# Kernel tuning notes

Measured on AMD Instinct MI355X. Metric: run time of the kernel, lower is better.

Reference implementation:

```python
import jax, jax.numpy as jnp
import numpy as np

B, T, D = 8, 2048, 512
S = 4                 # n_slots
SLOT_DIM = D          # cfg.slot_dim defaults to d_model
SE = 8                # state_embed_dim
GH = 64               # gate_hidden
EMA = 0.99
SIGMA_FLOOR = 1e-3
OPEN2CLOSING, CLOSING2LOCKED, UNLOCK = 0.1, 0.03, 0.25
GAINS = jnp.array([1.0, 0.5, 0.1], dtype=jnp.float32)  # OPEN, CLOSING, LOCKED


def _glorot(k, shape, fi, fo):
    b = (6.0 / (fi + fo)) ** 0.5
    return jax.random.uniform(k, shape, jnp.float32, -b, b)


def setup_inputs() -> dict:
    key = jax.random.key(0)
    ks = jax.random.split(key, 8)
    gate_in = D + 1 + SE  # [h, z, state_embed]
    return {
        'h_seq': jax.random.normal(ks[0], (B, T, D), jnp.float32),
        'pred_W': _glorot(ks[1], (S, D, D), D, D),
        'pred_b': jnp.zeros((S, D), jnp.float32),
        'gate_W1': _glorot(ks[2], (S, gate_in, GH), gate_in, GH),
        'gate_b1': jnp.zeros((S, GH), jnp.float32),
        'gate_W2': _glorot(ks[3], (S, GH, 1), GH, 1),
        'gate_b2': jnp.zeros((S, 1), jnp.float32),
        'write_W': _glorot(ks[4], (S, D, SLOT_DIM), D, SLOT_DIM),
        'write_b': jnp.zeros((S, SLOT_DIM), jnp.float32),
        'w0': jnp.zeros((S, SLOT_DIM), jnp.float32),
        'state_embed': jax.random.normal(ks[5], (3, SE), jnp.float32),
    }


def reference(h_seq, pred_W, pred_b, gate_W1, gate_b1, gate_W2, gate_b2,
              write_W, write_b, w0, state_embed):
    Bb, Tt, Dd = h_seq.shape
    h_det = jax.lax.stop_gradient(h_seq)
    # per-slot next-step predictions (input detached, as in torch): (B,T,S,D)
    preds = jnp.einsum('btd,sdo->btso', h_det, pred_W) + pred_b
    # prediction emitted at t-1 targets h_t
    pred_prev = jnp.concatenate([jnp.zeros_like(preds[:, :1]), preds[:, :-1]], axis=1)
    valid = jnp.arange(Tt) > 0  # no surprise signal at t=0

    m0 = jnp.broadcast_to(w0, (Bb, S, SLOT_DIM)).astype(h_seq.dtype)
    carry0 = (m0,
              jnp.zeros((S,), jnp.float32),       # mu
              jnp.ones((S,), jnp.float32),        # sigma
              jnp.full((S,), 0.5, jnp.float32),   # gate_ema
              jnp.zeros((S,), jnp.int32))         # slot_state

    def step(carry, xs):
        m, mu, sigma, gate_ema, state = carry
        h_t, p_prev, ok = xs  # (B,D), (B,S,D), scalar bool
        # prediction-error surprise per slot
        err = jnp.sqrt(jnp.sum((p_prev - h_t[:, None, :]) ** 2, axis=-1) + 1e-8)  # (B,S)
        err = jnp.where(ok, err, 0.0)
        z = (err - mu) / jnp.maximum(sigma, SIGMA_FLOOR)  # (B,S)
        # gate MLP over [h, z, state_embed]
        se = state_embed[state]  # (S,SE)
        gin = jnp.concatenate([
            jnp.broadcast_to(h_t[:, None, :], (Bb, S, Dd)),
            z[..., None],
            jnp.broadcast_to(se[None], (Bb, S, SE))], axis=-1)
        hid = jax.nn.relu(jnp.einsum('bsi,sih->bsh', gin, gate_W1) + gate_b1)
        g = jax.nn.sigmoid(jnp.einsum('bsh,sho->bso', hid, gate_W2) + gate_b2)[..., 0]  # (B,S)
        # state-dependent write gain (OPEN/CLOSING/LOCKED)
        g_eff = g * GAINS[state]
        w_enc = jnp.einsum('bd,sdo->bso', h_t, write_W) + write_b
        m = (1.0 - g_eff[..., None]) * m + g_eff[..., None] * w_enc
        read = m.reshape(Bb, S * SLOT_DIM)
        # homeostatic bookkeeping (buffers: non-differentiable, EMA)
        err_s = jax.lax.stop_gradient(err)
        mu_n = jnp.where(ok, EMA * mu + (1 - EMA) * err_s.mean(0), mu)
        sigma_n = jnp.where(ok, EMA * sigma + (1 - EMA) * jnp.abs(err_s - mu).mean(0), sigma)
        gate_ema_n = EMA * gate_ema + (1 - EMA) * jax.lax.stop_gradient(g).mean(0)
        # state machine transitions on gate EMA
        st = jnp.where((state == 0) & (gate_ema_n < OPEN2CLOSING), 1, state)
        st = jnp.where((state == 1) & (gate_ema_n < CLOSING2LOCKED), 2,
             jnp.where((state == 1) & (gate_ema_n > UNLOCK), 0, st))
        st = jnp.where((state == 2) & (gate_ema_n > UNLOCK), 0, st)
        return (m, mu_n, sigma_n, gate_ema_n, st), read

    xs = (jnp.swapaxes(h_seq, 0, 1), jnp.swapaxes(pred_prev, 0, 1), valid)
    _, reads = jax.lax.scan(step, carry0, xs)
    return jnp.swapaxes(reads, 0, 1)  # (B,T,S*SLOT_DIM)
```

## Files before the change

### kernel.cpp

```cpp
#include <hip/hip_runtime.h>
#include <hip/hip_bf16.h>

#define Bb 8
#define Tt 2048
#define Dd 512
#define Ss 4
#define GHh 64
#define NCHUNK 64
#define CH 32

typedef __hip_bfloat16 bf16;
typedef short bf16x8 __attribute__((ext_vector_type(8)));
typedef float f32x4 __attribute__((ext_vector_type(4)));
__device__ __forceinline__ float b2f(bf16 x){ return __bfloat162float(x); }

#define GLOAD_LDS16(g, l) \
  __builtin_amdgcn_global_load_lds((const __attribute__((address_space(1))) unsigned int*)(const void*)(g), \
                                   (__attribute__((address_space(3))) unsigned int*)(l), 16, 0, 0)

__global__ __launch_bounds__(256) void k0a_cvt(const float* __restrict__ h, bf16* __restrict__ hb){
  int i = (blockIdx.x*256 + threadIdx.x)*4;
  float4 v = *reinterpret_cast<const float4*>(&h[i]);
  hb[i+0] = __float2bfloat16(v.x);
  hb[i+1] = __float2bfloat16(v.y);
  hb[i+2] = __float2bfloat16(v.z);
  hb[i+3] = __float2bfloat16(v.w);
}

__global__ __launch_bounds__(256) void k0b_pack(const float* __restrict__ predW,
    const float* __restrict__ writeW, const float* __restrict__ gateW1, bf16* __restrict__ Wt){
  __shared__ float tile[32][33];
  int k0 = blockIdx.x*32, n0 = blockIdx.y*32;
  int tx = threadIdx.x & 31, ty = threadIdx.x >> 5;
  #pragma unroll
  for (int p = 0; p < 4; ++p) {
    int kk = ty + p*8;
    int n = n0 + tx, k = k0 + kk;
    float v;
    if (n < 2048)      { int s=n>>9, o=n&511;              v = predW[((size_t)s*512+k)*512+o]; }
    else if (n < 4096) { int n2=n-2048; int s=n2>>9,o=n2&511; v = writeW[((size_t)s*512+k)*512+o]; }
    else               { int n2=n-4096; int s=n2>>6,hh=n2&63; v = gateW1[((size_t)s*521+k)*64+hh]; }
    tile[kk][tx] = v;
  }
  __syncthreads();
  #pragma unroll
  for (int p = 0; p < 4; ++p) {
    int nn = ty + p*8;
    Wt[(size_t)(n0+nn)*512 + k0 + tx] = __float2bfloat16(tile[tx][nn]);
  }
}

__global__ __launch_bounds__(256) void k1_mfma(
    const bf16* __restrict__ hb, const bf16* __restrict__ Wt,
    const float* __restrict__ h, const float* __restrict__ predb, const float* __restrict__ writeb,
    bf16* __restrict__ wenc, float* __restrict__ hg, float* __restrict__ errsq)
{
  __shared__ bf16 As[2][128*64];
  __shared__ bf16 Bs[2][128*64];
  const int tid = threadIdx.x;
  const int w = tid >> 6, lane = tid & 63;
  const int n0 = blockIdx.x * 128;
  const int row0 = blockIdx.y * 128;
  const int wm = w & 1, wn = w >> 1;
  const int mrow = lane & 15, kq = lane >> 4;

  f32x4 acc[4][4];
  #pragma unroll
  for (int i=0;i<4;++i)
    #pragma unroll
    for (int j=0;j<4;++j) acc[i][j] = (f32x4){0.f,0.f,0.f,0.f};

  const int srow  = lane >> 3;
  const int sslot = (lane & 7) ^ srow;
  const bf16* gaBase = hb + (size_t)(row0 + w*32 + srow)*512 + sslot*8;
  const bf16* gbBase = Wt + (size_t)(n0  + w*32 + srow)*512 + sslot*8;

  auto STAGE = [&](int buf, int kstep){
    const bf16* ga = gaBase + kstep*64;
    const bf16* gb = gbBase + kstep*64;
    bf16* lA = &As[buf][(w*32)*64];
    bf16* lB = &Bs[buf][(w*32)*64];
    #pragma unroll
    for (int i=0;i<4;++i) {
      GLOAD_LDS16(ga + (size_t)i*8*512, lA + i*8*64);
      GLOAD_LDS16(gb + (size_t)i*8*512, lB + i*8*64);
    }
  };

  auto COMPUTE = [&](int buf){
    #pragma unroll
    for (int kk=0; kk<2; ++kk) {
      bf16x8 af[4], bfr[4];
      #pragma unroll
      for (int mi=0;mi<4;++mi) {
        int r = wm*64 + mi*16 + mrow;
        af[mi] = *reinterpret_cast<const bf16x8*>(&As[buf][r*64 + (((kk*4+kq) ^ (r&7))<<3)]);
      }
      #pragma unroll
      for (int ni=0;ni<4;++ni) {
        int r = wn*64 + ni*16 + mrow;
        bfr[ni] = *reinterpret_cast<const bf16x8*>(&Bs[buf][r*64 + (((kk*4+kq) ^ (r&7))<<3)]);
      }
      #pragma unroll
      for (int mi=0;mi<4;++mi)
        #pragma unroll
        for (int ni=0;ni<4;++ni)
          acc[mi][ni] = __builtin_amdgcn_mfma_f32_16x16x32_bf16(af[mi], bfr[ni], acc[mi][ni], 0, 0, 0);
    }
  };

  STAGE(0, 0);
  __syncthreads();
  #pragma unroll
  for (int t = 0; t < 8; ++t) {
    if (t < 7) STAGE((t+1)&1, t+1);
    COMPUTE(t&1);
    __syncthreads();
  }

  if (n0 < 2048) {
    const int s = n0 >> 9;
    #pragma unroll
    for (int mi=0;mi<4;++mi) {
      #pragma unroll
      for (int reg=0;reg<4;++reg) {
        int r = row0 + wm*64 + mi*16 + kq*4 + reg;
        float sum = 0.f;
        if ((r & 2047) != 2047) {
          #pragma unroll
          for (int ni=0;ni<4;++ni) {
            int o = (n0 & 511) + wn*64 + ni*16 + mrow;
            float P = acc[mi][ni][reg] + predb[s*512 + o];
            float d = P - h[(size_t)(r+1)*512 + o];
            sum = fmaf(d, d, sum);
          }
        }
        #pragma unroll
        for (int off=1; off<16; off<<=1) sum += __shfl_xor(sum, off);
        if (mrow == 0 && (r & 2047) != 2047)
          atomicAdd(&errsq[(size_t)(r+1)*4 + s], sum);
      }
    }
  } else if (n0 < 4096) {
    #pragma unroll
    for (int mi=0;mi<4;++mi)
      #pragma unroll
      for (int ni=0;ni<4;++ni) {
        int n2 = n0 - 2048 + wn*64 + ni*16 + mrow;
        int s = n2 >> 9, o = n2 & 511;
        float wb = writeb[s*512 + o];
        #pragma unroll
        for (int reg=0;reg<4;++reg) {
          int r = row0 + wm*64 + mi*16 + kq*4 + reg;
          wenc[((size_t)r*4 + s)*512 + o] = __float2bfloat16(acc[mi][ni][reg] + wb);
        }
      }
  } else {
    #pragma unroll
    for (int mi=0;mi<4;++mi)
      #pragma unroll
      for (int ni=0;ni<4;++ni) {
        int n2 = n0 - 4096 + wn*64 + ni*16 + mrow;
        int s = n2 >> 6, hh = n2 & 63;
        #pragma unroll
        for (int reg=0;reg<4;++reg) {
          int r = row0 + wm*64 + mi*16 + kq*4 + reg;
          hg[((size_t)r*4 + s)*64 + hh] = acc[mi][ni][reg];
        }
      }
  }
}

__global__ void k2a_err(const float* __restrict__ errsq, float* __restrict__ err){
  int i = blockIdx.x*256 + threadIdx.x;
  int t = (i >> 2) & 2047;
  err[i] = (t > 0) ? sqrtf(errsq[i] + 1e-8f) : 0.f;
}

__global__ void k2b_em(const float* __restrict__ err, float* __restrict__ em){
  int i = blockIdx.x*256 + threadIdx.x;
  float sum = 0.f;
  #pragma unroll
  for (int b=0;b<8;++b) sum += err[b*8192 + i];
  em[i] = sum * 0.125f;
}

__global__ void k2c_scan(const float* __restrict__ in, float* __restrict__ outv, float init){
  __shared__ float s_in[8192];
  for (int i = threadIdx.x; i < 8192; i += 256) s_in[i] = in[i];
  __syncthreads();
  if (threadIdx.x < 4) {
    int s = threadIdx.x;
    float v = init;
    for (int t = 0; t < 2048; ++t) {
      outv[t*4+s] = v;
      if (t >= 1) v = 0.99f*v + 0.01f*s_in[t*4+s];
    }
  }
}

__global__ void k2d_sd(const float* __restrict__ err, const float* __restrict__ MU, float* __restrict__ sd){
  int i = blockIdx.x*256 + threadIdx.x;
  float mu = MU[i];
  float sum = 0.f;
  #pragma unroll
  for (int b=0;b<8;++b) sum += fabsf(err[b*8192 + i] - mu);
  sd[i] = sum * 0.125f;
}

__global__ void k2e_base(const float* __restrict__ gateW1, const float* __restrict__ semb,
                         const float* __restrict__ gateb1, float* __restrict__ base1){
  int i = blockIdx.x*256 + threadIdx.x;
  if (i < 768) {
    int hh = i & 63, k = (i >> 6) % 3, s = i / 192;
    float acc = gateb1[s*64 + hh];
    #pragma unroll
    for (int e = 0; e < 8; ++e)
      acc = fmaf(semb[k*8+e], gateW1[((size_t)s*521 + 513 + e)*64 + hh], acc);
    base1[i] = acc;
  }
}

__global__ void k3_gall(const float* __restrict__ hg, const float* __restrict__ err,
    const float* __restrict__ MU, const float* __restrict__ SIG,
    const float* __restrict__ gateW1, const float* __restrict__ base1,
    const float* __restrict__ gateW2, const float* __restrict__ gateb2,
    float* __restrict__ g_all)
{
  int i = blockIdx.x*256 + threadIdx.x;
  int k = i % 3;
  int bts = i / 3;
  int s = bts & 3;
  int t = (bts >> 2) & 2047;
  float e = err[bts];
  float z = (e - MU[t*4+s]) / fmaxf(SIG[t*4+s], 1e-3f);
  const float* hgp = &hg[(size_t)bts*64];
  const float* b1p = &base1[(s*3 + k)*64];
  const float* w1zp = &gateW1[((size_t)s*521 + 512)*64];
  const float* w2p = &gateW2[s*64];
  float logit = 0.f;
  for (int hh = 0; hh < 64; ++hh) {
    float hid = hgp[hh] + z*w1zp[hh] + b1p[hh];
    hid = fmaxf(hid, 0.f);
    logit = fmaf(hid, w2p[hh], logit);
  }
  logit += gateb2[s];
  g_all[i] = 1.f/(1.f + expf(-logit));
}

__global__ void k3b_gm(const float* __restrict__ g_all, float* __restrict__ gm){
  int i = blockIdx.x*256 + threadIdx.x;
  float sum = 0.f;
  #pragma unroll
  for (int b=0;b<8;++b) sum += g_all[((size_t)b*8192 + i/3)*3 + (i%3)];
  gm[i] = sum * 0.125f;
}

__global__ void k4_scan(const float* __restrict__ gm, int* __restrict__ states){
  __shared__ float s_gm[6144];
  float ema = 0.5f; int st = 0;
  for (int c = 0; c < 4; ++c) {
    __syncthreads();
    for (int i = threadIdx.x; i < 6144; i += 256) s_gm[i] = gm[c*6144 + i];
    __syncthreads();
    if (threadIdx.x < 4) {
      int s = threadIdx.x;
      for (int tt = 0; tt < 512; ++tt) {
        int t = c*512 + tt;
        states[t*4+s] = st;
        float g = s_gm[tt*12 + s*3 + st];
        ema = 0.99f*ema + 0.01f*g;
        int ns = st;
        if (st == 0 && ema < 0.1f) ns = 1;
        if (st == 1) ns = (ema < 0.03f) ? 2 : ((ema > 0.25f) ? 0 : 1);
        if (st == 2 && ema > 0.25f) ns = 0;
        st = ns;
      }
    }
  }
}

__global__ void k5_a(const float* __restrict__ g_all, const int* __restrict__ states, float* __restrict__ a){
  int i = blockIdx.x*256 + threadIdx.x;
  int ts = i & 8191;
  int st = states[ts];
  float gain = (st == 0) ? 1.f : ((st == 1) ? 0.5f : 0.1f);
  a[i] = g_all[(size_t)i*3 + st] * gain;
}

__global__ __launch_bounds__(64) void k6_pass1(const float* __restrict__ a, const bf16* __restrict__ wenc,
      float* __restrict__ q, float* __restrict__ Pc){
  int c = blockIdx.x, s = blockIdx.y, b = blockIdx.z;
  int d0 = threadIdx.x << 3;
  __shared__ float s_a[CH];
  if (threadIdx.x < CH) s_a[threadIdx.x] = a[(size_t)(b*2048 + c*CH + threadIdx.x)*4 + s];
  __syncthreads();
  float qv[8];
  #pragma unroll
  for (int j=0;j<8;++j) qv[j] = 0.f;
  float p = 1.f;
  const bf16* wp = &wenc[((size_t)(b*2048 + c*CH)*4 + s)*512 + d0];
  #pragma unroll 4
  for (int i = 0; i < CH; ++i) {
    float av = s_a[i];
    bf16x8 wv = *reinterpret_cast<const bf16x8*>(wp + (size_t)i*4*512);
    float om = 1.f - av;
    #pragma unroll
    for (int j=0;j<8;++j) qv[j] = fmaf(om, qv[j], av*b2f(((const bf16*)&wv)[j]));
    p *= om;
  }
  float* qp = &q[((size_t)(b*4+s)*NCHUNK + c)*512 + d0];
  #pragma unroll
  for (int j=0;j<8;++j) qp[j] = qv[j];
  if (threadIdx.x == 0) Pc[(b*4+s)*NCHUNK + c] = p;
}

__global__ __launch_bounds__(512) void k7_bound(const float* __restrict__ q, const float* __restrict__ Pc,
      const float* __restrict__ w0, float* __restrict__ m_start){
  int s = blockIdx.x, b = blockIdx.y, d = threadIdx.x;
  float m = w0[s*512 + d];
  for (int c = 0; c < NCHUNK; ++c) {
    m_start[((size_t)(b*4+s)*NCHUNK + c)*512 + d] = m;
    m = Pc[(b*4+s)*NCHUNK + c]*m + q[((size_t)(b*4+s)*NCHUNK + c)*512 + d];
  }
}

__global__ __launch_bounds__(64) void k8_pass2(const float* __restrict__ a, const bf16* __restrict__ wenc,
      const float* __restrict__ m_start, float* __restrict__ out){
  int c = blockIdx.x, s = blockIdx.y, b = blockIdx.z;
  int d0 = threadIdx.x << 3;
  __shared__ float s_a[CH];
  if (threadIdx.x < CH) s_a[threadIdx.x] = a[(size_t)(b*2048 + c*CH + threadIdx.x)*4 + s];
  __syncthreads();
  float m[8];
  const float* msp = &m_start[((size_t)(b*4+s)*NCHUNK + c)*512 + d0];
  #pragma unroll
  for (int j=0;j<8;++j) m[j] = msp[j];
  const bf16* wp = &wenc[((size_t)(b*2048 + c*CH)*4 + s)*512 + d0];
  float* op = &out[((size_t)(b*2048 + c*CH))*2048 + s*512 + d0];
  #pragma unroll 2
  for (int i = 0; i < CH; ++i) {
    float av = s_a[i];
    bf16x8 wv = *reinterpret_cast<const bf16x8*>(wp + (size_t)i*4*512);
    float om = 1.f - av;
    #pragma unroll
    for (int j=0;j<8;++j) m[j] = fmaf(om, m[j], av*b2f(((const bf16*)&wv)[j]));
    #pragma unroll
    for (int j=0;j<8;++j) op[(size_t)i*2048 + j] = m[j];
  }
}

extern "C" void kernel_launch(void* const* d_in, const int* in_sizes, int n_in,
                              void* d_out, int out_size, void* d_ws, size_t ws_size,
                              hipStream_t stream) {
  (void)in_sizes; (void)n_in; (void)out_size; (void)ws_size;
  const float* h      = (const float*)d_in[0];
  const float* predW  = (const float*)d_in[1];
  const float* predb  = (const float*)d_in[2];
  const float* gateW1 = (const float*)d_in[3];
  const float* gateb1 = (const float*)d_in[4];
  const float* gateW2 = (const float*)d_in[5];
  const float* gateb2 = (const float*)d_in[6];
  const float* writeW = (const float*)d_in[7];
  const float* writeb = (const float*)d_in[8];
  const float* w0     = (const float*)d_in[9];
  const float* semb   = (const float*)d_in[10];
  float* out = (float*)d_out;

  char* ws = (char*)d_ws;
  size_t off = 0;
  auto alloc = [&](size_t bytes) -> char* {
    char* p = ws + off; off += (bytes + 255) / 256 * 256; return p;
  };
  bf16*  wenc   = (bf16*) alloc((size_t)Bb*Tt*Ss*Dd*2);
  float* hg     = (float*)alloc((size_t)Bb*Tt*Ss*GHh*4);
  bf16*  hb     = (bf16*) alloc((size_t)Bb*Tt*Dd*2);
  bf16*  Wt     = (bf16*) alloc((size_t)4352*512*2);
  float* errsq  = (float*)alloc((size_t)Bb*Tt*Ss*4);
  float* err    = (float*)alloc((size_t)Bb*Tt*Ss*4);
  float* em     = (float*)alloc((size_t)Tt*Ss*4);
  float* MU     = (float*)alloc((size_t)Tt*Ss*4);
  float* sd     = (float*)alloc((size_t)Tt*Ss*4);
  float* SIG    = (float*)alloc((size_t)Tt*Ss*4);
  float* base1  = (float*)alloc((size_t)Ss*3*GHh*4);
  float* g_all  = (float*)alloc((size_t)Bb*Tt*Ss*3*4);
  float* gm     = (float*)alloc((size_t)Tt*Ss*3*4);
  int*   states = (int*)  alloc((size_t)Tt*Ss*4);
  float* av     = (float*)alloc((size_t)Bb*Tt*Ss*4);
  float* Pc     = (float*)alloc((size_t)Bb*Ss*NCHUNK*4);
  float* q      = (float*)alloc((size_t)Bb*Ss*NCHUNK*Dd*4);
  float* mst    = (float*)alloc((size_t)Bb*Ss*NCHUNK*Dd*4);

  hipMemsetAsync(errsq, 0, (size_t)Bb*Tt*Ss*4, stream);

  k0a_cvt<<<(Bb*Tt*Dd)/(256*4), 256, 0, stream>>>(h, hb);
  dim3 g0b(16, 136);
  k0b_pack<<<g0b, 256, 0, stream>>>(predW, writeW, gateW1, Wt);
  dim3 g1(34, 128);
  k1_mfma<<<g1, 256, 0, stream>>>(hb, Wt, h, predb, writeb, wenc, hg, errsq);
  k2a_err<<<(Bb*Tt*Ss)/256, 256, 0, stream>>>(errsq, err);
  k2b_em<<<(Tt*Ss)/256, 256, 0, stream>>>(err, em);
  k2c_scan<<<1, 256, 0, stream>>>(em, MU, 0.f);
  k2d_sd<<<(Tt*Ss)/256, 256, 0, stream>>>(err, MU, sd);
  k2c_scan<<<1, 256, 0, stream>>>(sd, SIG, 1.f);
  k2e_base<<<3, 256, 0, stream>>>(gateW1, semb, gateb1, base1);
  k3_gall<<<(Bb*Tt*Ss*3)/256, 256, 0, stream>>>(hg, err, MU, SIG, gateW1, base1, gateW2, gateb2, g_all);
  k3b_gm<<<(Tt*Ss*3)/256, 256, 0, stream>>>(g_all, gm);
  k4_scan<<<1, 256, 0, stream>>>(gm, states);
  k5_a<<<(Bb*Tt*Ss)/256, 256, 0, stream>>>(g_all, states, av);
  dim3 g6(NCHUNK, Ss, Bb);
  k6_pass1<<<g6, 64, 0, stream>>>(av, wenc, q, Pc);
  dim3 g7(Ss, Bb);
  k7_bound<<<g7, 512, 0, stream>>>(q, Pc, w0, mst);
  k8_pass2<<<g6, 64, 0, stream>>>(av, wenc, mst, out);
}
```

Before: 646.5 us.

## Parallelize EMA scan into chunks and shorten state-machine dependency chain

The mu/sigma EMA scan kernel becomes a three-phase chunked linear scan: 256 threads each reduce a 32-step chunk to an affine (A,B) pair, four threads combine the chunk prefixes, then every thread replays its chunk to write outputs. This replaces a 2048-step serial loop that ran on four threads. The gate-EMA state-machine scan, which must stay serial, now double-buffers its shared-memory staging so the next chunk loads while the current one runs. Its loop body computes all three candidate EMAs and next states before selecting, which takes the branchy state-dependent load off the critical path. Computing A as a power of 0.99 and reordering the FMAs may change float rounding slightly.

```diff
diff --git a/kernel.cpp b/kernel.cpp
--- a/kernel.cpp
+++ b/kernel.cpp
@@ -185,17 +185,35 @@
   em[i] = sum * 0.125f;
 }
 
-__global__ void k2c_scan(const float* __restrict__ in, float* __restrict__ outv, float init){
+__global__ __launch_bounds__(256) void k2c_scan(const float* __restrict__ in, float* __restrict__ outv, float init){
   __shared__ float s_in[8192];
+  __shared__ float sA[256], sB[256], s_entry[256];
   for (int i = threadIdx.x; i < 8192; i += 256) s_in[i] = in[i];
   __syncthreads();
+  const int c = threadIdx.x >> 2, s = threadIdx.x & 3;
+  float A = 1.f, B = 0.f;
+  #pragma unroll 8
+  for (int i = 0; i < 32; ++i) {
+    int t = c*32 + i;
+    if (t >= 1) { A *= 0.99f; B = fmaf(0.99f, B, 0.01f * s_in[t*4 + s]); }
+  }
+  sA[threadIdx.x] = A; sB[threadIdx.x] = B;
+  __syncthreads();
   if (threadIdx.x < 4) {
-    int s = threadIdx.x;
+    int ss = threadIdx.x;
     float v = init;
-    for (int t = 0; t < 2048; ++t) {
-      outv[t*4+s] = v;
-      if (t >= 1) v = 0.99f*v + 0.01f*s_in[t*4+s];
+    for (int cc = 0; cc < 64; ++cc) {
+      s_entry[cc*4 + ss] = v;
+      v = fmaf(sA[cc*4 + ss], v, sB[cc*4 + ss]);
     }
+  }
+  __syncthreads();
+  float v = s_entry[threadIdx.x];
+  #pragma unroll 8
+  for (int i = 0; i < 32; ++i) {
+    int t = c*32 + i;
+    outv[t*4 + s] = v;
+    if (t >= 1) v = fmaf(0.99f, v, 0.01f * s_in[t*4 + s]);
   }
 }
 
@@ -256,27 +274,34 @@
   gm[i] = sum * 0.125f;
 }
 
-__global__ void k4_scan(const float* __restrict__ gm, int* __restrict__ states){
-  __shared__ float s_gm[6144];
+__global__ __launch_bounds__(256) void k4_scan(const float* __restrict__ gm, int* __restrict__ states){
+  __shared__ float s_gm[2][6144];
+  for (int i = threadIdx.x; i < 6144; i += 256) s_gm[0][i] = gm[i];
+  __syncthreads();
   float ema = 0.5f; int st = 0;
   for (int c = 0; c < 4; ++c) {
-    __syncthreads();
-    for (int i = threadIdx.x; i < 6144; i += 256) s_gm[i] = gm[c*6144 + i];
-    __syncthreads();
+    if (c < 3)
+      for (int i = threadIdx.x; i < 6144; i += 256) s_gm[(c+1)&1][i] = gm[(c+1)*6144 + i];
     if (threadIdx.x < 4) {
       int s = threadIdx.x;
+      const float* gp = &s_gm[c&1][s*3];
+      int* sp = &states[c*2048 + s];
+      #pragma unroll 8
       for (int tt = 0; tt < 512; ++tt) {
-        int t = c*512 + tt;
-        states[t*4+s] = st;
-        float g = s_gm[tt*12 + s*3 + st];
-        ema = 0.99f*ema + 0.01f*g;
-        int ns = st;
-        if (st == 0 && ema < 0.1f) ns = 1;
-        if (st == 1) ns = (ema < 0.03f) ? 2 : ((ema > 0.25f) ? 0 : 1);
-        if (st == 2 && ema > 0.25f) ns = 0;
-        st = ns;
+        sp[tt*4] = st;
+        float g0 = gp[tt*12+0], g1 = gp[tt*12+1], g2 = gp[tt*12+2];
+        float base = 0.99f * ema;
+        float e0 = fmaf(0.01f, g0, base);
+        float e1 = fmaf(0.01f, g1, base);
+        float e2 = fmaf(0.01f, g2, base);
+        ema = (st == 0) ? e0 : ((st == 1) ? e1 : e2);
+        int n0 = (ema < 0.1f) ? 1 : 0;
+        int n1 = (ema < 0.03f) ? 2 : ((ema > 0.25f) ? 0 : 1);
+        int n2 = (ema > 0.25f) ? 0 : 2;
+        st = (st == 0) ? n0 : ((st == 1) ? n1 : n2);
       }
     }
+    __syncthreads();
   }
 }
 
```

Result: faster. 546.4 us (-15.5%).
